# Performance work log

Measured on AMD Instinct MI355X. Metric: run time of the kernel, lower is better.

## Reference

```python
import jax, jax.numpy as jnp
import numpy as np
import math

B, L, D = 2, 2048, 512
H, HD = 8, 64                      # num_heads, head_dim = D // H
NG = D * (D - 1) // 2              # SO(D) generator count = 130816


def setup_inputs() -> dict:
    key = jax.random.key(0)
    ks = jax.random.split(key, 8)
    x = jax.random.normal(ks[0], (B, L, D), jnp.float32)
    # additive causal mask [L, L]
    mask = jnp.where(jnp.tril(jnp.ones((L, L), bool)), 0.0, -1e9).astype(jnp.float32)
    coef = lambda k: jax.random.normal(k, (NG,), jnp.float32) * 0.1
    basis = lambda k: jax.random.normal(k, (HD, HD), jnp.float32) * 0.1
    return {
        "x": x, "mask": mask,
        "coef_q": coef(ks[1]), "coef_k": coef(ks[2]),
        "coef_v": coef(ks[3]), "coef_o": coef(ks[4]),
        "bias_q": jnp.zeros((D,), jnp.float32), "bias_k": jnp.zeros((D,), jnp.float32),
        "bias_v": jnp.zeros((D,), jnp.float32), "bias_o": jnp.zeros((D,), jnp.float32),
        "basis_q": basis(ks[5]), "basis_k": basis(ks[6]),
    }


def _make_W(coefs):
    # W = I + sum_i coef_i * G_i, with G_i the antisymmetric basis (row-major i<j).
    iu = jnp.triu_indices(D, k=1)
    A = jnp.zeros((D, D), coefs.dtype).at[iu].set(coefs)
    return A - A.T + jnp.eye(D, dtype=coefs.dtype)


def _proj(x, coefs, bias):
    # F.linear(x, W, b) = x @ W.T + b
    return x @ _make_W(coefs).T + bias


def _invariants(t, basis):
    # t: [B, H, L, HD] -> concat(norm, t @ basis.T)[..., :HD]
    norm = jnp.linalg.norm(t, axis=-1, keepdims=True)
    ip = jnp.einsum('bhld,nd->bhln', t, basis)
    return jnp.concatenate([norm, ip], axis=-1)[..., :HD]


def reference(x, mask, coef_q, coef_k, coef_v, coef_o,
              bias_q, bias_k, bias_v, bias_o, basis_q, basis_k):
    split = lambda t: t.reshape(B, L, H, HD).transpose(0, 2, 1, 3)  # [B,H,L,HD]
    Q = split(_proj(x, coef_q, bias_q))
    K = split(_proj(x, coef_k, bias_k))
    V = split(_proj(x, coef_v, bias_v))
    Qi = _invariants(Q, basis_q)
    Ki = _invariants(K, basis_k)
    scores = jnp.einsum('bhld,bhmd->bhlm', Qi, Ki) / math.sqrt(HD) + mask
    attn = jax.nn.softmax(scores, axis=-1)
    out = jnp.einsum('bhlm,bhmd->bhld', attn, V)
    out = out.transpose(0, 2, 1, 3).reshape(B, L, D)
    return _proj(out, coef_o, bias_o)
```

## Files before the change

kernel.cpp:

```cpp
#include <hip/hip_runtime.h>
#include <hip/hip_bf16.h>
#include <math.h>

#define D_ 512
#define B_ 2
#define L_ 2048
#define H_ 8
#define HD_ 64

typedef __attribute__((ext_vector_type(8))) short short8;
typedef __attribute__((ext_vector_type(4))) float f32x4;
typedef _Float16 half8 __attribute__((ext_vector_type(8)));

__device__ __forceinline__ ushort f2bf(float f) {
  __hip_bfloat16 h = __float2bfloat16(f);
  return *(ushort*)&h;
}
__device__ __forceinline__ float bf2f(ushort u) {
  unsigned int v = ((unsigned int)u) << 16;
  union { unsigned int u; float f; } c; c.u = v; return c.f;
}
__device__ __forceinline__ ushort f2h(float f) {
  _Float16 h = (_Float16)f;
  return *(ushort*)&h;
}
__device__ __forceinline__ int swz(int row, int col) {
  return row*64 + (((col>>3) ^ (row&7))<<3) + (col&7);
}
__device__ __forceinline__ int tri_idx(int i, int j) {
  return i*(D_-1) - (i*(i-1))/2 + (j - i - 1);
}

#define GLL16(g, l) __builtin_amdgcn_global_load_lds( \
    (const __attribute__((address_space(1))) void*)(g), \
    (__attribute__((address_space(3))) void*)(l), 16, 0, 0)

__global__ void prep_kernel(const float* __restrict__ x,
                            const float* __restrict__ cq, const float* __restrict__ ck,
                            const float* __restrict__ cv, const float* __restrict__ co,
                            const float* __restrict__ basq, const float* __restrict__ bask,
                            ushort* __restrict__ xb, ushort* __restrict__ Wb,
                            ushort* __restrict__ Bq, ushort* __restrict__ Bk) {
  int blk = blockIdx.x, tid = threadIdx.x;
  if (blk < 2048) {
    int i = (blk*256 + tid)*4;
    float4 v = *(const float4*)(x + i);
    ushort4 o = make_ushort4(f2h(v.x), f2h(v.y), f2h(v.z), f2h(v.w));
    *(ushort4*)(xb + i) = o;
  } else if (blk < 6144) {
    int e = (blk-2048)*256 + tid;
    int m = e >> 18, n = (e>>9)&511, k = e&511;
    const float* cf = (m==0)?cq:(m==1)?ck:(m==2)?cv:co;
    float v = (k>n) ? cf[tri_idx(n,k)] : (k<n) ? -cf[tri_idx(k,n)] : 0.f;
    Wb[e] = f2h(v);
  } else {
    int e = (blk-6144)*256 + tid;
    int which = e >> 12, ee = e & 4095;
    int n = ee >> 6, d = ee & 63;
    const float* bs = which ? bask : basq;
    float v = (n==0) ? 0.f : bs[(n-1)*64 + d];
    (which ? Bk : Bq)[ee] = f2h(v);
  }
}

__device__ __forceinline__ void stage_xw(const ushort* __restrict__ Xg,
                                         const ushort* __restrict__ Wqg,
                                         const ushort* __restrict__ Wkg,
                                         const ushort* __restrict__ Wvg,
                                         ushort* A, ushort* Q, ushort* K, ushort* V,
                                         int w, int lane) {
  const int r8 = lane >> 3;
  const int cx = (lane & 7) ^ r8;
  #pragma unroll
  for (int s = 0; s < 2; ++s) {
    const int seg = w*2 + s;
    const int row = seg*8 + r8;
    const size_t go = (size_t)row*512 + cx*8;
    GLL16(Xg  + go, (char*)A + seg*1024);
    GLL16(Wqg + go, (char*)Q + seg*1024);
    GLL16(Wkg + go, (char*)K + seg*1024);
    GLL16(Wvg + go, (char*)V + seg*1024);
  }
}

__global__ __launch_bounds__(256) void proj_qkv_kernel(
    const ushort* __restrict__ Xb, const float* __restrict__ Xf,
    const ushort* __restrict__ Wb,
    const float* __restrict__ bq, const float* __restrict__ bk,
    const float* __restrict__ bv,
    const ushort* __restrict__ Bq, const ushort* __restrict__ Bk,
    ushort* __restrict__ QiO, float* __restrict__ NqV,
    ushort* __restrict__ KiO, float* __restrict__ NkV,
    ushort* __restrict__ Vt_g, float* __restrict__ TileMax)
{
  __shared__ ushort BufA[2][4096];
  __shared__ ushort BufQ[2][4096];
  __shared__ ushort BufK[2][4096];
  __shared__ ushort BufV[2][4096];
  __shared__ float WaveMax[4];

  const int tid = threadIdx.x;
  const int lane = tid & 63, w = tid >> 6;
  const int lr = lane & 15, lg = lane >> 4;
  const int h = blockIdx.x, mb = blockIdx.y;
  const int n0 = h*64, m0 = mb*64;
  const ushort* Xg  = Xb + (size_t)m0*512;
  const ushort* Wqg = Wb + (size_t)n0*512;
  const ushort* Wkg = Wb + 262144 + (size_t)n0*512;
  const ushort* Wvg = Wb + 524288 + (size_t)n0*512;

  f32x4 accQ[4] = {}, accK[4] = {}, accV[4] = {};
  stage_xw(Xg, Wqg, Wkg, Wvg, BufA[0], BufQ[0], BufK[0], BufV[0], w, lane);

  for (int p = 0; p < 8; ++p) {
    const int cur = p & 1;
    if (p < 7) {
      const int k0 = (p+1)*64;
      stage_xw(Xg + k0, Wqg + k0, Wkg + k0, Wvg + k0,
               BufA[cur^1], BufQ[cur^1], BufK[cur^1], BufV[cur^1], w, lane);
      asm volatile("s_waitcnt vmcnt(8)" ::: "memory");
    } else {
      asm volatile("s_waitcnt vmcnt(0)" ::: "memory");
    }
    __builtin_amdgcn_sched_barrier(0);
    __builtin_amdgcn_s_barrier();
    __builtin_amdgcn_sched_barrier(0);

    half8 af[2];
    #pragma unroll
    for (int ks = 0; ks < 2; ++ks)
      af[ks] = *(const half8*)&BufA[cur][swz(w*16+lr, (ks*4+lg)*8)];
    #pragma unroll
    for (int nb = 0; nb < 4; ++nb) {
      #pragma unroll
      for (int ks = 0; ks < 2; ++ks) {
        int so = swz(nb*16+lr, (ks*4+lg)*8);
        accQ[nb] = __builtin_amdgcn_mfma_f32_16x16x32_f16(af[ks], *(const half8*)&BufQ[cur][so], accQ[nb], 0,0,0);
        accK[nb] = __builtin_amdgcn_mfma_f32_16x16x32_f16(af[ks], *(const half8*)&BufK[cur][so], accK[nb], 0,0,0);
        accV[nb] = __builtin_amdgcn_mfma_f32_16x16x32_f16(af[ks], *(const half8*)&BufV[cur][so], accV[nb], 0,0,0);
      }
    }
    __builtin_amdgcn_sched_barrier(0);
    __builtin_amdgcn_s_barrier();
    __builtin_amdgcn_sched_barrier(0);
  }

  float ex[4][4];
  #pragma unroll
  for (int nb = 0; nb < 4; ++nb)
    #pragma unroll
    for (int r = 0; r < 4; ++r) {
      size_t m = m0 + w*16 + lg*4 + r;
      ex[nb][r] = Xf[m*512 + n0 + nb*16 + lr];
    }
  const int b = m0 >> 11;

  #pragma unroll
  for (int nb = 0; nb < 4; ++nb) {
    float bv4 = bv[n0 + nb*16 + lr];
    float v0 = ex[nb][0] + accV[nb][0] + bv4;
    float v1 = ex[nb][1] + accV[nb][1] + bv4;
    float v2 = ex[nb][2] + accV[nb][2] + bv4;
    float v3 = ex[nb][3] + accV[nb][3] + bv4;
    ushort4 o = make_ushort4(f2bf(v0), f2bf(v1), f2bf(v2), f2bf(v3));
    int l0 = (m0 & 2047) + w*16 + lg*4;
    size_t idx = (size_t)(b*8 + h)*131072 + (size_t)(nb*16 + lr)*2048 + l0;
    *(ushort4*)(Vt_g + idx) = o;
  }

  float qQ[4][4], qK[4][4];
  #pragma unroll
  for (int nb = 0; nb < 4; ++nb) {
    float bq4 = bq[n0 + nb*16 + lr];
    float bk4 = bk[n0 + nb*16 + lr];
    #pragma unroll
    for (int r = 0; r < 4; ++r) {
      qQ[nb][r] = ex[nb][r] + accQ[nb][r] + bq4;
      qK[nb][r] = ex[nb][r] + accK[nb][r] + bk4;
    }
  }
  float normQ[4], normK[4];
  #pragma unroll
  for (int r = 0; r < 4; ++r) {
    float sq = 0.f, sk = 0.f;
    #pragma unroll
    for (int nb = 0; nb < 4; ++nb) {
      sq = fmaf(qQ[nb][r], qQ[nb][r], sq);
      sk = fmaf(qK[nb][r], qK[nb][r], sk);
    }
    sq += __shfl_xor(sq, 1, 16); sk += __shfl_xor(sk, 1, 16);
    sq += __shfl_xor(sq, 2, 16); sk += __shfl_xor(sk, 2, 16);
    sq += __shfl_xor(sq, 4, 16); sk += __shfl_xor(sk, 4, 16);
    sq += __shfl_xor(sq, 8, 16); sk += __shfl_xor(sk, 8, 16);
    normQ[r] = sqrtf(sq); normK[r] = sqrtf(sk);
  }
  __syncthreads();
  {
    #pragma unroll
    for (int i = 0; i < 2; ++i) {
      int idx = tid + 256*i;
      int row = idx >> 3, c = idx & 7;
      int so = swz(row, c*8);
      *(short8*)&BufQ[0][so] = *(const short8*)(Bq + row*64 + c*8);
      *(short8*)&BufK[0][so] = *(const short8*)(Bk + row*64 + c*8);
    }
  }
  #pragma unroll
  for (int nb = 0; nb < 4; ++nb)
    #pragma unroll
    for (int r = 0; r < 4; ++r) {
      int so = swz(w*16 + lg*4 + r, nb*16 + lr);
      BufA[0][so] = f2h(qQ[nb][r]);
      BufV[0][so] = f2h(qK[nb][r]);
    }
  __syncthreads();

  f32x4 acc2Q[4] = {}, acc2K[4] = {};
  half8 aq[2], ak[2];
  #pragma unroll
  for (int ks = 0; ks < 2; ++ks) {
    aq[ks] = *(const half8*)&BufA[0][swz(w*16+lr, (ks*4+lg)*8)];
    ak[ks] = *(const half8*)&BufV[0][swz(w*16+lr, (ks*4+lg)*8)];
  }
  #pragma unroll
  for (int nb = 0; nb < 4; ++nb) {
    #pragma unroll
    for (int ks = 0; ks < 2; ++ks) {
      int so = swz(nb*16+lr, (ks*4+lg)*8);
      acc2Q[nb] = __builtin_amdgcn_mfma_f32_16x16x32_f16(aq[ks], *(const half8*)&BufQ[0][so], acc2Q[nb], 0,0,0);
      acc2K[nb] = __builtin_amdgcn_mfma_f32_16x16x32_f16(ak[ks], *(const half8*)&BufK[0][so], acc2K[nb], 0,0,0);
    }
  }

  float rnq[4] = {0.f,0.f,0.f,0.f}, rnk[4] = {0.f,0.f,0.f,0.f};
  #pragma unroll
  for (int nb = 0; nb < 4; ++nb)
    #pragma unroll
    for (int r = 0; r < 4; ++r) {
      int ninv = nb*16 + lr;
      int l = (m0 & 2047) + w*16 + lg*4 + r;
      float vq = (ninv == 0) ? normQ[r] : acc2Q[nb][r];
      vq *= 0.125f;
      rnq[r] = fmaf(vq, vq, rnq[r]);
      QiO[((size_t)(b*8 + h)*2048 + l)*64 + ninv] = f2h(vq);
      float vk = (ninv == 0) ? normK[r] : acc2K[nb][r];
      rnk[r] = fmaf(vk, vk, rnk[r]);
      KiO[((size_t)(b*8 + h)*2048 + l)*64 + ninv] = f2h(vk);
    }
  float kmax = -1e30f;
  #pragma unroll
  for (int r = 0; r < 4; ++r) {
    float sq = rnq[r], sk = rnk[r];
    sq += __shfl_xor(sq, 1, 16); sk += __shfl_xor(sk, 1, 16);
    sq += __shfl_xor(sq, 2, 16); sk += __shfl_xor(sk, 2, 16);
    sq += __shfl_xor(sq, 4, 16); sk += __shfl_xor(sk, 4, 16);
    sq += __shfl_xor(sq, 8, 16); sk += __shfl_xor(sk, 8, 16);
    float nk = sqrtf(sk);
    kmax = fmaxf(kmax, nk);
    if (lr == 0) {
      int l = (m0 & 2047) + w*16 + lg*4 + r;
      NqV[(size_t)(b*8 + h)*2048 + l] = sqrtf(sq);
      NkV[(size_t)(b*8 + h)*2048 + l] = nk;
    }
  }
  kmax = fmaxf(kmax, __shfl_xor(kmax, 16));
  kmax = fmaxf(kmax, __shfl_xor(kmax, 32));
  if (lane == 0) WaveMax[w] = kmax;
  __syncthreads();
  if (tid == 0) {
    float m01 = fmaxf(WaveMax[0], WaveMax[1]);
    float m23 = fmaxf(WaveMax[2], WaveMax[3]);
    TileMax[(b*8 + h)*32 + (mb & 31)] = fmaxf(m01, m23);
  }
}

__device__ __forceinline__ void stage_kv(const ushort* __restrict__ Kg,
                                         const ushort* __restrict__ Vg,
                                         ushort* KB, ushort* VB,
                                         int w, int lane) {
  const int r8 = lane >> 3;
  const int cx = (lane & 7) ^ r8;
  #pragma unroll
  for (int s = 0; s < 2; ++s) {
    const int seg = w*2 + s;
    const int row = seg*8 + r8;
    GLL16(Kg + (size_t)row*64 + cx*8,   (char*)KB + seg*1024);
    GLL16(Vg + (size_t)row*2048 + cx*8, (char*)VB + seg*1024);
  }
}

__global__ __launch_bounds__(256) void attn_kernel(
    const ushort* __restrict__ Qi_g, const float* __restrict__ NqV,
    const ushort* __restrict__ Ki_g, const float* __restrict__ TileMax,
    const ushort* __restrict__ Vt_g,
    float* __restrict__ PartO, float* __restrict__ PartL)
{
  __shared__ ushort KS[2][4096], VS[2][4096], Pl[4096];

  const int tid = threadIdx.x;
  const int lane = tid & 63, w = tid >> 6;
  const int lr = lane & 15, lg = lane >> 4;
  const int blk = blockIdx.x;
  const int bh = ((blk & 7) << 1) | ((blk >> 3) & 1);
  const int gh = blk >> 4;
  const int g  = gh & 31;
  const int half = gh >> 5;
  const int qb = (g < 16) ? (31 - g) : (g - 16);
  const int T = qb + 1, mid = (T + 1) >> 1;
  const int lo = half ? mid : 0, hi = half ? T : mid;
  const ushort* Kg0 = Ki_g + (size_t)bh*131072;
  const ushort* Vg0 = Vt_g + (size_t)bh*131072;
  const int qg0 = qb*64;
  const int qloc = w*16 + lr;
  const int prow = qloc;

  const size_t qoff = ((size_t)bh*2048 + qg0 + qloc)*64;
  const half8 qf0 = *(const half8*)(Qi_g + qoff + lg*8);
  const half8 qf1 = *(const half8*)(Qi_g + qoff + 32 + lg*8);
  const float nqv = NqV[(size_t)bh*2048 + qg0 + qloc];

  float mk = (lane <= qb) ? TileMax[bh*32 + lane] : -1e30f;
  #pragma unroll
  for (int off = 1; off < 64; off <<= 1) mk = fmaxf(mk, __shfl_xor(mk, off));
  const float m_ub = nqv * mk;

  float l_lane = 0.f;
  f32x4 accO[4] = {};

  if (lo < hi)
    stage_kv(Kg0 + (size_t)lo*4096, Vg0 + lo*64, KS[lo&1], VS[lo&1], w, lane);

  for (int jb = lo; jb < hi; ++jb) {
    const int cur = jb & 1;
    if (jb + 1 < hi) {
      stage_kv(Kg0 + (size_t)(jb+1)*4096, Vg0 + (jb+1)*64,
               KS[cur^1], VS[cur^1], w, lane);
      asm volatile("s_waitcnt vmcnt(4)" ::: "memory");
    } else {
      asm volatile("s_waitcnt vmcnt(0)" ::: "memory");
    }
    __builtin_amdgcn_sched_barrier(0);
    __builtin_amdgcn_s_barrier();
    __builtin_amdgcn_sched_barrier(0);

    f32x4 sf[4];
    #pragma unroll
    for (int cb = 0; cb < 4; ++cb) {
      f32x4 a = {0.f,0.f,0.f,0.f};
      half8 k0 = *(const half8*)&KS[cur][swz(cb*16+lr, lg*8)];
      half8 k1 = *(const half8*)&KS[cur][swz(cb*16+lr, (4+lg)*8)];
      a = __builtin_amdgcn_mfma_f32_16x16x32_f16(k0, qf0, a, 0,0,0);
      a = __builtin_amdgcn_mfma_f32_16x16x32_f16(k1, qf1, a, 0,0,0);
      sf[cb] = a;
    }
    if (jb == qb) {
      #pragma unroll
      for (int cb = 0; cb < 4; ++cb)
        #pragma unroll
        for (int r = 0; r < 4; ++r)
          if (cb*16 + lg*4 + r > qloc) sf[cb][r] = -1e30f;
    }

    #pragma unroll
    for (int cb = 0; cb < 4; ++cb)
      #pragma unroll
      for (int r = 0; r < 4; ++r) {
        float p = __expf(sf[cb][r] - m_ub);
        l_lane += p;
        sf[cb][r] = p;
      }
    #pragma unroll
    for (int cb = 0; cb < 4; ++cb) {
      ushort4 pk = make_ushort4(f2bf(sf[cb][0]), f2bf(sf[cb][1]),
                                f2bf(sf[cb][2]), f2bf(sf[cb][3]));
      *(ushort4*)&Pl[swz(prow, cb*16 + lg*4)] = pk;
    }

    short8 pfr[2];
    #pragma unroll
    for (int ks = 0; ks < 2; ++ks)
      pfr[ks] = *(const short8*)&Pl[swz(prow, (ks*4+lg)*8)];
    #pragma unroll
    for (int db = 0; db < 4; ++db) {
      f32x4 a = accO[db];
      short8 v0 = *(const short8*)&VS[cur][swz(db*16+lr, lg*8)];
      short8 v1 = *(const short8*)&VS[cur][swz(db*16+lr, (4+lg)*8)];
      a = __builtin_amdgcn_mfma_f32_16x16x32_bf16(v0, pfr[0], a, 0,0,0);
      a = __builtin_amdgcn_mfma_f32_16x16x32_bf16(v1, pfr[1], a, 0,0,0);
      accO[db] = a;
    }

    __builtin_amdgcn_sched_barrier(0);
    __builtin_amdgcn_s_barrier();
    __builtin_amdgcn_sched_barrier(0);
  }

  l_lane += __shfl_xor(l_lane, 16);
  l_lane += __shfl_xor(l_lane, 32);
  const int pbase = half*512 + bh*32 + qb;
  #pragma unroll
  for (int db = 0; db < 4; ++db)
    *(f32x4*)(PartO + (size_t)pbase*4096 + qloc*64 + db*16 + lg*4) = accO[db];
  if (lg == 0) PartL[pbase*64 + qloc] = l_lane;
}

__global__ __launch_bounds__(256) void proj_o_kernel(
    const float* __restrict__ PartO, const float* __restrict__ PartL,
    const ushort* __restrict__ Wb, const float* __restrict__ bo,
    float* __restrict__ OutF)
{
  __shared__ ushort BufA[4096];
  __shared__ ushort BufB[4096];
  __shared__ float ExactT[64][65];

  const int tid = threadIdx.x;
  const int lane = tid & 63, w = tid >> 6;
  const int lr = lane & 15, lg = lane >> 4;
  const int h = blockIdx.x, mb = blockIdx.y;
  const int n0 = h*64, m0 = mb*64;
  const ushort* Wm = Wb + 3*262144;
  const int b_ = m0 >> 11;
  const int qb_ = (m0 & 2047) >> 6;

  float4 r0a[2], r0b[2], r1a[2], r1b[2];
  float rl0[2], rl1[2];
  short8 rw[2];

  auto issue = [&](int p) {
    const int bh_ = b_*8 + p;
    const size_t pb0 = (size_t)(bh_*32 + qb_)*4096;
    const int lbase = (bh_*32 + qb_)*64;
    #pragma unroll
    for (int i = 0; i < 2; ++i) {
      int idx = tid + 256*i;
      int row = idx >> 3, c = idx & 7;
      rl0[i] = PartL[lbase + row];
      rl1[i] = PartL[32768 + lbase + row];
      const float* s0 = PartO + pb0 + row*64 + c*8;
      r0a[i] = *(const float4*)s0;
      r0b[i] = *(const float4*)(s0 + 4);
      r1a[i] = *(const float4*)(s0 + 2097152);
      r1b[i] = *(const float4*)(s0 + 2097152 + 4);
      rw[i] = *(const short8*)(Wm + (size_t)(n0+row)*512 + p*64 + c*8);
    }
  };

  issue(0);
  f32x4 acc[4] = {};
  for (int p = 0; p < 8; ++p) {
    __syncthreads();
    #pragma unroll
    for (int i = 0; i < 2; ++i) {
      int idx = tid + 256*i;
      int row = idx >> 3, c = idx & 7;
      float inv = 1.0f / (rl0[i] + rl1[i]);
      float o[8] = {(r0a[i].x+r1a[i].x)*inv, (r0a[i].y+r1a[i].y)*inv,
                    (r0a[i].z+r1a[i].z)*inv, (r0a[i].w+r1a[i].w)*inv,
                    (r0b[i].x+r1b[i].x)*inv, (r0b[i].y+r1b[i].y)*inv,
                    (r0b[i].z+r1b[i].z)*inv, (r0b[i].w+r1b[i].w)*inv};
      if (p == h) {
        #pragma unroll
        for (int k = 0; k < 8; ++k) ExactT[row][c*8+k] = o[k];
      }
      ushort u[8];
      #pragma unroll
      for (int k = 0; k < 8; ++k) u[k] = f2h(o[k]);
      *(short8*)&BufA[swz(row, c*8)] = *(short8*)u;
      *(short8*)&BufB[swz(row, c*8)] = rw[i];
    }
    if (p < 7) issue(p+1);
    __syncthreads();
    half8 af[2];
    #pragma unroll
    for (int ks = 0; ks < 2; ++ks)
      af[ks] = *(const half8*)&BufA[swz(w*16+lr, (ks*4+lg)*8)];
    #pragma unroll
    for (int nb = 0; nb < 4; ++nb) {
      #pragma unroll
      for (int ks = 0; ks < 2; ++ks) {
        half8 bfr = *(const half8*)&BufB[swz(nb*16+lr, (ks*4+lg)*8)];
        acc[nb] = __builtin_amdgcn_mfma_f32_16x16x32_f16(af[ks], bfr, acc[nb], 0,0,0);
      }
    }
  }

  #pragma unroll
  for (int nb = 0; nb < 4; ++nb) {
    float bo4 = bo[n0 + nb*16 + lr];
    #pragma unroll
    for (int r = 0; r < 4; ++r) {
      int row = w*16 + lg*4 + r;
      size_t m = m0 + row;
      OutF[m*512 + n0 + nb*16 + lr] = ExactT[row][nb*16 + lr] + acc[nb][r] + bo4;
    }
  }
}

extern "C" void kernel_launch(void* const* d_in, const int* in_sizes, int n_in,
                              void* d_out, int out_size, void* d_ws, size_t ws_size,
                              hipStream_t stream) {
  const float* x       = (const float*)d_in[0];
  const float* coef_q  = (const float*)d_in[2];
  const float* coef_k  = (const float*)d_in[3];
  const float* coef_v  = (const float*)d_in[4];
  const float* coef_o  = (const float*)d_in[5];
  const float* bias_q  = (const float*)d_in[6];
  const float* bias_k  = (const float*)d_in[7];
  const float* bias_v  = (const float*)d_in[8];
  const float* bias_o  = (const float*)d_in[9];
  const float* basis_q = (const float*)d_in[10];
  const float* basis_k = (const float*)d_in[11];
  float* out = (float*)d_out;

  ushort* xb    = (ushort*)d_ws;
  ushort* Wb    = xb + 2097152;
  ushort* Bq    = Wb + 1048576;
  ushort* Bk    = Bq + 4096;
  ushort* Qi    = Bk + 4096;
  ushort* Ki    = Qi + 2097152;
  ushort* Vt_g  = Ki + 2097152;
  float*  NqV   = (float*)(Vt_g + 2097152);
  float*  NkV   = NqV + 32768;
  float*  PartO = NkV + 32768;
  float*  PartL = PartO + 4194304;
  float*  TileMax = PartL + 65536;

  prep_kernel<<<dim3(6176), 256, 0, stream>>>(x, coef_q, coef_k, coef_v, coef_o,
                                              basis_q, basis_k, xb, Wb, Bq, Bk);

  proj_qkv_kernel<<<dim3(8, 64), 256, 0, stream>>>(xb, x, Wb,
      bias_q, bias_k, bias_v, Bq, Bk, Qi, NqV, Ki, NkV, Vt_g, TileMax);

  attn_kernel<<<dim3(1024), 256, 0, stream>>>(Qi, NqV, Ki, TileMax, Vt_g,
                                              PartO, PartL);

  proj_o_kernel<<<dim3(8, 64), 256, 0, stream>>>(PartO, PartL, Wb, bias_o, out);
}
```

Baseline: 75.99 us.

## Process two KV tiles per iteration with a four-deep shared-memory ring

The attention loop now handles two 64-key tiles per iteration and keeps four KV buffers in LDS, prefetching two tiles ahead. This halves the number of block-wide barriers per key and gives the scheduler two independent score/exp chains to interleave, aiming to hide load and MFMA latency. In exchange, LDS use roughly doubles (about 72KB per block), which can lower occupancy, and register pressure rises. An odd remaining tile is handled in a separate tail.

```diff
diff --git a/kernel.cpp b/kernel.cpp
--- a/kernel.cpp
+++ b/kernel.cpp
@@ -295,7 +295,7 @@
     const ushort* __restrict__ Vt_g,
     float* __restrict__ PartO, float* __restrict__ PartL)
 {
-  __shared__ ushort KS[2][4096], VS[2][4096], Pl[4096];
+  __shared__ ushort KS[4][4096], VS[4][4096], Pl[4096];
 
   const int tid = threadIdx.x;
   const int lane = tid & 63, w = tid >> 6;
@@ -328,27 +328,137 @@
   f32x4 accO[4] = {};
 
   if (lo < hi)
-    stage_kv(Kg0 + (size_t)lo*4096, Vg0 + lo*64, KS[lo&1], VS[lo&1], w, lane);
-
-  for (int jb = lo; jb < hi; ++jb) {
-    const int cur = jb & 1;
-    if (jb + 1 < hi) {
-      stage_kv(Kg0 + (size_t)(jb+1)*4096, Vg0 + (jb+1)*64,
-               KS[cur^1], VS[cur^1], w, lane);
-      asm volatile("s_waitcnt vmcnt(4)" ::: "memory");
-    } else {
-      asm volatile("s_waitcnt vmcnt(0)" ::: "memory");
-    }
+    stage_kv(Kg0 + (size_t)lo*4096, Vg0 + lo*64, KS[lo&3], VS[lo&3], w, lane);
+  if (lo + 1 < hi)
+    stage_kv(Kg0 + (size_t)(lo+1)*4096, Vg0 + (lo+1)*64,
+             KS[(lo+1)&3], VS[(lo+1)&3], w, lane);
+
+  int jb = lo;
+  for (; jb + 1 < hi; jb += 2) {
+    int nst = 0;
+    if (jb + 2 < hi) {
+      stage_kv(Kg0 + (size_t)(jb+2)*4096, Vg0 + (jb+2)*64,
+               KS[(jb+2)&3], VS[(jb+2)&3], w, lane);
+      ++nst;
+    }
+    if (jb + 3 < hi) {
+      stage_kv(Kg0 + (size_t)(jb+3)*4096, Vg0 + (jb+3)*64,
+               KS[(jb+3)&3], VS[(jb+3)&3], w, lane);
+      ++nst;
+    }
+    if (nst == 2)      asm volatile("s_waitcnt vmcnt(8)" ::: "memory");
+    else if (nst == 1) asm volatile("s_waitcnt vmcnt(4)" ::: "memory");
+    else               asm volatile("s_waitcnt vmcnt(0)" ::: "memory");
     __builtin_amdgcn_sched_barrier(0);
     __builtin_amdgcn_s_barrier();
     __builtin_amdgcn_sched_barrier(0);
 
-    f32x4 sf[4];
+    const ushort* KA = KS[jb & 3];
+    const ushort* VA = VS[jb & 3];
+    const ushort* KB = KS[(jb+1) & 3];
+    const ushort* VB = VS[(jb+1) & 3];
+
+    f32x4 sfA[4], sfB[4];
     #pragma unroll
     for (int cb = 0; cb < 4; ++cb) {
       f32x4 a = {0.f,0.f,0.f,0.f};
-      half8 k0 = *(const half8*)&KS[cur][swz(cb*16+lr, lg*8)];
-      half8 k1 = *(const half8*)&KS[cur][swz(cb*16+lr, (4+lg)*8)];
+      half8 k0 = *(const half8*)&KA[swz(cb*16+lr, lg*8)];
+      half8 k1 = *(const half8*)&KA[swz(cb*16+lr, (4+lg)*8)];
+      a = __builtin_amdgcn_mfma_f32_16x16x32_f16(k0, qf0, a, 0,0,0);
+      a = __builtin_amdgcn_mfma_f32_16x16x32_f16(k1, qf1, a, 0,0,0);
+      sfA[cb] = a;
+      f32x4 b2 = {0.f,0.f,0.f,0.f};
+      half8 k2 = *(const half8*)&KB[swz(cb*16+lr, lg*8)];
+      half8 k3 = *(const half8*)&KB[swz(cb*16+lr, (4+lg)*8)];
+      b2 = __builtin_amdgcn_mfma_f32_16x16x32_f16(k2, qf0, b2, 0,0,0);
+      b2 = __builtin_amdgcn_mfma_f32_16x16x32_f16(k3, qf1, b2, 0,0,0);
+      sfB[cb] = b2;
+    }
+    if (jb == qb) {
+      #pragma unroll
+      for (int cb = 0; cb < 4; ++cb)
+        #pragma unroll
+        for (int r = 0; r < 4; ++r)
+          if (cb*16 + lg*4 + r > qloc) sfA[cb][r] = -1e30f;
+    }
+    if (jb + 1 == qb) {
+      #pragma unroll
+      for (int cb = 0; cb < 4; ++cb)
+        #pragma unroll
+        for (int r = 0; r < 4; ++r)
+          if (cb*16 + lg*4 + r > qloc) sfB[cb][r] = -1e30f;
+    }
+
+    #pragma unroll
+    for (int cb = 0; cb < 4; ++cb)
+      #pragma unroll
+      for (int r = 0; r < 4; ++r) {
+        float p = __expf(sfA[cb][r] - m_ub);
+        l_lane += p;
+        sfA[cb][r] = p;
+      }
+    #pragma unroll
+    for (int cb = 0; cb < 4; ++cb)
+      #pragma unroll
+      for (int r = 0; r < 4; ++r) {
+        float p = __expf(sfB[cb][r] - m_ub);
+        l_lane += p;
+        sfB[cb][r] = p;
+      }
+
+    #pragma unroll
+    for (int cb = 0; cb < 4; ++cb) {
+      ushort4 pk = make_ushort4(f2bf(sfA[cb][0]), f2bf(sfA[cb][1]),
+                                f2bf(sfA[cb][2]), f2bf(sfA[cb][3]));
+      *(ushort4*)&Pl[swz(prow, cb*16 + lg*4)] = pk;
+    }
+    short8 pfrA[2];
+    #pragma unroll
+    for (int ks = 0; ks < 2; ++ks)
+      pfrA[ks] = *(const short8*)&Pl[swz(prow, (ks*4+lg)*8)];
+    #pragma unroll
+    for (int cb = 0; cb < 4; ++cb) {
+      ushort4 pk = make_ushort4(f2bf(sfB[cb][0]), f2bf(sfB[cb][1]),
+                                f2bf(sfB[cb][2]), f2bf(sfB[cb][3]));
+      *(ushort4*)&Pl[swz(prow, cb*16 + lg*4)] = pk;
+    }
+    short8 pfrB[2];
+    #pragma unroll
+    for (int ks = 0; ks < 2; ++ks)
+      pfrB[ks] = *(const short8*)&Pl[swz(prow, (ks*4+lg)*8)];
+
+    #pragma unroll
+    for (int db = 0; db < 4; ++db) {
+      f32x4 a = accO[db];
+      short8 v0 = *(const short8*)&VA[swz(db*16+lr, lg*8)];
+      short8 v1 = *(const short8*)&VA[swz(db*16+lr, (4+lg)*8)];
+      a = __builtin_amdgcn_mfma_f32_16x16x32_bf16(v0, pfrA[0], a, 0,0,0);
+      a = __builtin_amdgcn_mfma_f32_16x16x32_bf16(v1, pfrA[1], a, 0,0,0);
+      short8 v2 = *(const short8*)&VB[swz(db*16+lr, lg*8)];
+      short8 v3 = *(const short8*)&VB[swz(db*16+lr, (4+lg)*8)];
+      a = __builtin_amdgcn_mfma_f32_16x16x32_bf16(v2, pfrB[0], a, 0,0,0);
+      a = __builtin_amdgcn_mfma_f32_16x16x32_bf16(v3, pfrB[1], a, 0,0,0);
+      accO[db] = a;
+    }
+
+    __builtin_amdgcn_sched_barrier(0);
+    __builtin_amdgcn_s_barrier();
+    __builtin_amdgcn_sched_barrier(0);
+  }
+
+  if (jb < hi) {
+    asm volatile("s_waitcnt vmcnt(0)" ::: "memory");
+    __builtin_amdgcn_sched_barrier(0);
+    __builtin_amdgcn_s_barrier();
+    __builtin_amdgcn_sched_barrier(0);
+    const ushort* KA = KS[jb & 3];
+    const ushort* VA = VS[jb & 3];
+    f32x4 sf[4];
+    #pragma unroll
+    for (int cb = 0; cb < 4; ++cb) {
+      f32x4 a = {0.f,0.f,0.f,0.f};
+      half8 k0 = *(const half8*)&KA[swz(cb*16+lr, lg*8)];
+      half8 k1 = *(const half8*)&KA[swz(cb*16+lr, (4+lg)*8)];
       a = __builtin_amdgcn_mfma_f32_16x16x32_f16(k0, qf0, a, 0,0,0);
       a = __builtin_amdgcn_mfma_f32_16x16x32_f16(k1, qf1, a, 0,0,0);
       sf[cb] = a;
@@ -360,7 +470,6 @@
         for (int r = 0; r < 4; ++r)
           if (cb*16 + lg*4 + r > qloc) sf[cb][r] = -1e30f;
     }
-
     #pragma unroll
     for (int cb = 0; cb < 4; ++cb)
       #pragma unroll
@@ -375,7 +484,6 @@
                                 f2bf(sf[cb][2]), f2bf(sf[cb][3]));
       *(ushort4*)&Pl[swz(prow, cb*16 + lg*4)] = pk;
     }
-
     short8 pfr[2];
     #pragma unroll
     for (int ks = 0; ks < 2; ++ks)
@@ -383,16 +491,12 @@
     #pragma unroll
     for (int db = 0; db < 4; ++db) {
       f32x4 a = accO[db];
-      short8 v0 = *(const short8*)&VS[cur][swz(db*16+lr, lg*8)];
-      short8 v1 = *(const short8*)&VS[cur][swz(db*16+lr, (4+lg)*8)];
+      short8 v0 = *(const short8*)&VA[swz(db*16+lr, lg*8)];
+      short8 v1 = *(const short8*)&VA[swz(db*16+lr, (4+lg)*8)];
       a = __builtin_amdgcn_mfma_f32_16x16x32_bf16(v0, pfr[0], a, 0,0,0);
       a = __builtin_amdgcn_mfma_f32_16x16x32_bf16(v1, pfr[1], a, 0,0,0);
       accO[db] = a;
     }
-
-    __builtin_amdgcn_sched_barrier(0);
-    __builtin_amdgcn_s_barrier();
-    __builtin_amdgcn_sched_barrier(0);
   }
 
   l_lane += __shfl_xor(l_lane, 16);
```

Result: no change. 76.75 us (+1.0%).

## Share staged K/V tiles across two query blocks per 512-thread workgroup

Applied to the files above, without the earlier changes.

The attention kernel now runs 512 threads per block. Each block handles a pair of adjacent 64-row query blocks (8 waves), and both share the same double-buffered K/V tiles in shared memory, which roughly halves the K/V global loads and LDS staging per query row. The split into two partial halves is re-derived per pair, and the lower query block masks out tiles beyond its diagonal. Those masked tiles still cost full MFMA work and barriers, and the larger blocks reduce the count of independent workgroups.

```diff
diff --git a/kernel.cpp b/kernel.cpp
--- a/kernel.cpp
+++ b/kernel.cpp
@@ -274,52 +274,48 @@
   }
 }
 
-__device__ __forceinline__ void stage_kv(const ushort* __restrict__ Kg,
-                                         const ushort* __restrict__ Vg,
-                                         ushort* KB, ushort* VB,
-                                         int w, int lane) {
+__device__ __forceinline__ void stage_kv8(const ushort* __restrict__ Kg,
+                                          const ushort* __restrict__ Vg,
+                                          ushort* KB, ushort* VB,
+                                          int w, int lane) {
   const int r8 = lane >> 3;
   const int cx = (lane & 7) ^ r8;
-  #pragma unroll
-  for (int s = 0; s < 2; ++s) {
-    const int seg = w*2 + s;
-    const int row = seg*8 + r8;
-    GLL16(Kg + (size_t)row*64 + cx*8,   (char*)KB + seg*1024);
-    GLL16(Vg + (size_t)row*2048 + cx*8, (char*)VB + seg*1024);
-  }
-}
-
-__global__ __launch_bounds__(256) void attn_kernel(
+  const int row = w*8 + r8;
+  GLL16(Kg + (size_t)row*64 + cx*8,   (char*)KB + w*1024);
+  GLL16(Vg + (size_t)row*2048 + cx*8, (char*)VB + w*1024);
+}
+
+__global__ __launch_bounds__(512) void attn_kernel(
     const ushort* __restrict__ Qi_g, const float* __restrict__ NqV,
     const ushort* __restrict__ Ki_g, const float* __restrict__ TileMax,
     const ushort* __restrict__ Vt_g,
     float* __restrict__ PartO, float* __restrict__ PartL)
 {
-  __shared__ ushort KS[2][4096], VS[2][4096], Pl[4096];
+  __shared__ ushort KS[2][4096], VS[2][4096], Pl[8][1024];
 
   const int tid = threadIdx.x;
   const int lane = tid & 63, w = tid >> 6;
   const int lr = lane & 15, lg = lane >> 4;
   const int blk = blockIdx.x;
   const int bh = ((blk & 7) << 1) | ((blk >> 3) & 1);
-  const int gh = blk >> 4;
-  const int g  = gh & 31;
-  const int half = gh >> 5;
-  const int qb = (g < 16) ? (31 - g) : (g - 16);
-  const int T = qb + 1, mid = (T + 1) >> 1;
-  const int lo = half ? mid : 0, hi = half ? T : mid;
+  const int rest = blk >> 4;
+  const int rr = rest & 15;
+  const int half = rest >> 4;
+  const int qt = half ? (15 - rr) : rr;
+  const int qbw = 2*qt + (w >> 2);
+  const int lo = half ? (qt + 1) : 0;
+  const int hi = half ? (2*qt + 2) : (qt + 1);
   const ushort* Kg0 = Ki_g + (size_t)bh*131072;
   const ushort* Vg0 = Vt_g + (size_t)bh*131072;
-  const int qg0 = qb*64;
-  const int qloc = w*16 + lr;
-  const int prow = qloc;
-
-  const size_t qoff = ((size_t)bh*2048 + qg0 + qloc)*64;
+  const int qloc = (w & 3)*16 + lr;
+  ushort* Plw = Pl[w];
+
+  const size_t qoff = ((size_t)bh*2048 + qbw*64 + qloc)*64;
   const half8 qf0 = *(const half8*)(Qi_g + qoff + lg*8);
   const half8 qf1 = *(const half8*)(Qi_g + qoff + 32 + lg*8);
-  const float nqv = NqV[(size_t)bh*2048 + qg0 + qloc];
-
-  float mk = (lane <= qb) ? TileMax[bh*32 + lane] : -1e30f;
+  const float nqv = NqV[(size_t)bh*2048 + qbw*64 + qloc];
+
+  float mk = (lane <= qbw) ? TileMax[bh*32 + lane] : -1e30f;
   #pragma unroll
   for (int off = 1; off < 64; off <<= 1) mk = fmaxf(mk, __shfl_xor(mk, off));
   const float m_ub = nqv * mk;
@@ -328,14 +324,14 @@
   f32x4 accO[4] = {};
 
   if (lo < hi)
-    stage_kv(Kg0 + (size_t)lo*4096, Vg0 + lo*64, KS[lo&1], VS[lo&1], w, lane);
+    stage_kv8(Kg0 + (size_t)lo*4096, Vg0 + lo*64, KS[lo&1], VS[lo&1], w, lane);
 
   for (int jb = lo; jb < hi; ++jb) {
     const int cur = jb & 1;
     if (jb + 1 < hi) {
-      stage_kv(Kg0 + (size_t)(jb+1)*4096, Vg0 + (jb+1)*64,
-               KS[cur^1], VS[cur^1], w, lane);
-      asm volatile("s_waitcnt vmcnt(4)" ::: "memory");
+      stage_kv8(Kg0 + (size_t)(jb+1)*4096, Vg0 + (jb+1)*64,
+                KS[cur^1], VS[cur^1], w, lane);
+      asm volatile("s_waitcnt vmcnt(2)" ::: "memory");
     } else {
       asm volatile("s_waitcnt vmcnt(0)" ::: "memory");
     }
@@ -353,12 +349,18 @@
       a = __builtin_amdgcn_mfma_f32_16x16x32_f16(k1, qf1, a, 0,0,0);
       sf[cb] = a;
     }
-    if (jb == qb) {
+    if (jb == qbw) {
       #pragma unroll
       for (int cb = 0; cb < 4; ++cb)
         #pragma unroll
         for (int r = 0; r < 4; ++r)
           if (cb*16 + lg*4 + r > qloc) sf[cb][r] = -1e30f;
+    } else if (jb > qbw) {
+      #pragma unroll
+      for (int cb = 0; cb < 4; ++cb)
+        #pragma unroll
+        for (int r = 0; r < 4; ++r)
+          sf[cb][r] = -1e30f;
     }
 
     #pragma unroll
@@ -373,13 +375,13 @@
     for (int cb = 0; cb < 4; ++cb) {
       ushort4 pk = make_ushort4(f2bf(sf[cb][0]), f2bf(sf[cb][1]),
                                 f2bf(sf[cb][2]), f2bf(sf[cb][3]));
-      *(ushort4*)&Pl[swz(prow, cb*16 + lg*4)] = pk;
+      *(ushort4*)&Plw[swz(lr, cb*16 + lg*4)] = pk;
     }
 
     short8 pfr[2];
     #pragma unroll
     for (int ks = 0; ks < 2; ++ks)
-      pfr[ks] = *(const short8*)&Pl[swz(prow, (ks*4+lg)*8)];
+      pfr[ks] = *(const short8*)&Plw[swz(lr, (ks*4+lg)*8)];
     #pragma unroll
     for (int db = 0; db < 4; ++db) {
       f32x4 a = accO[db];
@@ -397,7 +399,7 @@
 
   l_lane += __shfl_xor(l_lane, 16);
   l_lane += __shfl_xor(l_lane, 32);
-  const int pbase = half*512 + bh*32 + qb;
+  const int pbase = half*512 + bh*32 + qbw;
   #pragma unroll
   for (int db = 0; db < 4; ++db)
     *(f32x4*)(PartO + (size_t)pbase*4096 + qloc*64 + db*16 + lg*4) = accO[db];
@@ -531,8 +533,8 @@
   proj_qkv_kernel<<<dim3(8, 64), 256, 0, stream>>>(xb, x, Wb,
       bias_q, bias_k, bias_v, Bq, Bk, Qi, NqV, Ki, NkV, Vt_g, TileMax);
 
-  attn_kernel<<<dim3(1024), 256, 0, stream>>>(Qi, NqV, Ki, TileMax, Vt_g,
-                                              PartO, PartL);
+  attn_kernel<<<dim3(512), 512, 0, stream>>>(Qi, NqV, Ki, TileMax, Vt_g,
+                                             PartO, PartL);
 
   proj_o_kernel<<<dim3(8, 64), 256, 0, stream>>>(PartO, PartL, Wb, bias_o, out);
 }
```

New measurement: 76.21 us. About the same (+0.3%).

## Run attention blocks as single wave handling all 64 query rows

Applied to the files above, without the earlier changes.

The attention kernel drops from four waves per block to one wave that processes all four 16-row query slices. K/V fragments are loaded into registers once per tile and reused across the four slices, and the per-tile block barriers are removed because one wave does all the staging and compute. In exchange, register pressure rises a lot (16 accumulator tiles plus 16 score tiles), which may cut occupancy or cause spills. Each block now has a quarter of the threads to issue loads and hide latency, and LDS per block is unchanged.

```diff
diff --git a/kernel.cpp b/kernel.cpp
--- a/kernel.cpp
+++ b/kernel.cpp
@@ -274,31 +274,28 @@
   }
 }
 
-__device__ __forceinline__ void stage_kv(const ushort* __restrict__ Kg,
-                                         const ushort* __restrict__ Vg,
-                                         ushort* KB, ushort* VB,
-                                         int w, int lane) {
+__device__ __forceinline__ void stage_kv1(const ushort* __restrict__ Kg,
+                                          const ushort* __restrict__ Vg,
+                                          ushort* KB, ushort* VB, int lane) {
   const int r8 = lane >> 3;
   const int cx = (lane & 7) ^ r8;
   #pragma unroll
-  for (int s = 0; s < 2; ++s) {
-    const int seg = w*2 + s;
+  for (int seg = 0; seg < 8; ++seg) {
     const int row = seg*8 + r8;
     GLL16(Kg + (size_t)row*64 + cx*8,   (char*)KB + seg*1024);
     GLL16(Vg + (size_t)row*2048 + cx*8, (char*)VB + seg*1024);
   }
 }
 
-__global__ __launch_bounds__(256) void attn_kernel(
+__global__ __launch_bounds__(64) void attn_kernel(
     const ushort* __restrict__ Qi_g, const float* __restrict__ NqV,
     const ushort* __restrict__ Ki_g, const float* __restrict__ TileMax,
     const ushort* __restrict__ Vt_g,
     float* __restrict__ PartO, float* __restrict__ PartL)
 {
-  __shared__ ushort KS[2][4096], VS[2][4096], Pl[4096];
-
-  const int tid = threadIdx.x;
-  const int lane = tid & 63, w = tid >> 6;
+  __shared__ ushort KS[2][4096], VS[2][4096], Pl[4][1024];
+
+  const int lane = threadIdx.x & 63;
   const int lr = lane & 15, lg = lane >> 4;
   const int blk = blockIdx.x;
   const int bh = ((blk & 7) << 1) | ((blk >> 3) & 1);
@@ -310,98 +307,116 @@
   const int lo = half ? mid : 0, hi = half ? T : mid;
   const ushort* Kg0 = Ki_g + (size_t)bh*131072;
   const ushort* Vg0 = Vt_g + (size_t)bh*131072;
-  const int qg0 = qb*64;
-  const int qloc = w*16 + lr;
-  const int prow = qloc;
-
-  const size_t qoff = ((size_t)bh*2048 + qg0 + qloc)*64;
-  const half8 qf0 = *(const half8*)(Qi_g + qoff + lg*8);
-  const half8 qf1 = *(const half8*)(Qi_g + qoff + 32 + lg*8);
-  const float nqv = NqV[(size_t)bh*2048 + qg0 + qloc];
+
+  half8 qf[4][2];
+  float nqv[4];
+  #pragma unroll
+  for (int i = 0; i < 4; ++i) {
+    const size_t qoff = ((size_t)bh*2048 + qb*64 + i*16 + lr)*64;
+    qf[i][0] = *(const half8*)(Qi_g + qoff + lg*8);
+    qf[i][1] = *(const half8*)(Qi_g + qoff + 32 + lg*8);
+    nqv[i] = NqV[(size_t)bh*2048 + qb*64 + i*16 + lr];
+  }
 
   float mk = (lane <= qb) ? TileMax[bh*32 + lane] : -1e30f;
   #pragma unroll
   for (int off = 1; off < 64; off <<= 1) mk = fmaxf(mk, __shfl_xor(mk, off));
-  const float m_ub = nqv * mk;
-
-  float l_lane = 0.f;
-  f32x4 accO[4] = {};
+  float m_ub[4];
+  #pragma unroll
+  for (int i = 0; i < 4; ++i) m_ub[i] = nqv[i] * mk;
+
+  float l[4] = {0.f, 0.f, 0.f, 0.f};
+  f32x4 accO[4][4] = {};
 
   if (lo < hi)
-    stage_kv(Kg0 + (size_t)lo*4096, Vg0 + lo*64, KS[lo&1], VS[lo&1], w, lane);
+    stage_kv1(Kg0 + (size_t)lo*4096, Vg0 + lo*64, KS[lo&1], VS[lo&1], lane);
 
   for (int jb = lo; jb < hi; ++jb) {
     const int cur = jb & 1;
     if (jb + 1 < hi) {
-      stage_kv(Kg0 + (size_t)(jb+1)*4096, Vg0 + (jb+1)*64,
-               KS[cur^1], VS[cur^1], w, lane);
-      asm volatile("s_waitcnt vmcnt(4)" ::: "memory");
+      stage_kv1(Kg0 + (size_t)(jb+1)*4096, Vg0 + (jb+1)*64,
+                KS[cur^1], VS[cur^1], lane);
+      asm volatile("s_waitcnt vmcnt(16)" ::: "memory");
     } else {
       asm volatile("s_waitcnt vmcnt(0)" ::: "memory");
     }
     __builtin_amdgcn_sched_barrier(0);
-    __builtin_amdgcn_s_barrier();
-    __builtin_amdgcn_sched_barrier(0);
-
-    f32x4 sf[4];
+
+    half8 kf[4][2];
+    short8 vf[4][2];
     #pragma unroll
     for (int cb = 0; cb < 4; ++cb) {
-      f32x4 a = {0.f,0.f,0.f,0.f};
-      half8 k0 = *(const half8*)&KS[cur][swz(cb*16+lr, lg*8)];
-      half8 k1 = *(const half8*)&KS[cur][swz(cb*16+lr, (4+lg)*8)];
-      a = __builtin_amdgcn_mfma_f32_16x16x32_f16(k0, qf0, a, 0,0,0);
-      a = __builtin_amdgcn_mfma_f32_16x16x32_f16(k1, qf1, a, 0,0,0);
-      sf[cb] = a;
-    }
+      kf[cb][0] = *(const half8*)&KS[cur][swz(cb*16+lr, lg*8)];
+      kf[cb][1] = *(const half8*)&KS[cur][swz(cb*16+lr, (4+lg)*8)];
+      vf[cb][0] = *(const short8*)&VS[cur][swz(cb*16+lr, lg*8)];
+      vf[cb][1] = *(const short8*)&VS[cur][swz(cb*16+lr, (4+lg)*8)];
+    }
+
+    f32x4 sf[4][4];
+    #pragma unroll
+    for (int i = 0; i < 4; ++i)
+      #pragma unroll
+      for (int cb = 0; cb < 4; ++cb) {
+        f32x4 a = {0.f,0.f,0.f,0.f};
+        a = __builtin_amdgcn_mfma_f32_16x16x32_f16(kf[cb][0], qf[i][0], a, 0,0,0);
+        a = __builtin_amdgcn_mfma_f32_16x16x32_f16(kf[cb][1], qf[i][1], a, 0,0,0);
+        sf[i][cb] = a;
+      }
     if (jb == qb) {
+      #pragma unroll
+      for (int i = 0; i < 4; ++i)
+        #pragma unroll
+        for (int cb = 0; cb < 4; ++cb)
+          #pragma unroll
+          for (int r = 0; r < 4; ++r)
+            if (cb*16 + lg*4 + r > i*16 + lr) sf[i][cb][r] = -1e30f;
+    }
+
+    #pragma unroll
+    for (int i = 0; i < 4; ++i)
       #pragma unroll
       for (int cb = 0; cb < 4; ++cb)
         #pragma unroll
-        for (int r = 0; r < 4; ++r)
-          if (cb*16 + lg*4 + r > qloc) sf[cb][r] = -1e30f;
-    }
-
-    #pragma unroll
-    for (int cb = 0; cb < 4; ++cb)
-      #pragma unroll
-      for (int r = 0; r < 4; ++r) {
-        float p = __expf(sf[cb][r] - m_ub);
-        l_lane += p;
-        sf[cb][r] = p;
+        for (int r = 0; r < 4; ++r) {
+          float p = __expf(sf[i][cb][r] - m_ub[i]);
+          l[i] += p;
+          sf[i][cb][r] = p;
+        }
+
+    #pragma unroll
+    for (int i = 0; i < 4; ++i)
+      #pragma unroll
+      for (int cb = 0; cb < 4; ++cb) {
+        ushort4 pk = make_ushort4(f2bf(sf[i][cb][0]), f2bf(sf[i][cb][1]),
+                                  f2bf(sf[i][cb][2]), f2bf(sf[i][cb][3]));
+        *(ushort4*)&Pl[i][swz(lr, cb*16 + lg*4)] = pk;
       }
     #pragma unroll
-    for (int cb = 0; cb < 4; ++cb) {
-      ushort4 pk = make_ushort4(f2bf(sf[cb][0]), f2bf(sf[cb][1]),
-                                f2bf(sf[cb][2]), f2bf(sf[cb][3]));
-      *(ushort4*)&Pl[swz(prow, cb*16 + lg*4)] = pk;
-    }
-
-    short8 pfr[2];
-    #pragma unroll
-    for (int ks = 0; ks < 2; ++ks)
-      pfr[ks] = *(const short8*)&Pl[swz(prow, (ks*4+lg)*8)];
-    #pragma unroll
-    for (int db = 0; db < 4; ++db) {
-      f32x4 a = accO[db];
-      short8 v0 = *(const short8*)&VS[cur][swz(db*16+lr, lg*8)];
-      short8 v1 = *(const short8*)&VS[cur][swz(db*16+lr, (4+lg)*8)];
-      a = __builtin_amdgcn_mfma_f32_16x16x32_bf16(v0, pfr[0], a, 0,0,0);
-      a = __builtin_amdgcn_mfma_f32_16x16x32_bf16(v1, pfr[1], a, 0,0,0);
-      accO[db] = a;
-    }
-
-    __builtin_amdgcn_sched_barrier(0);
-    __builtin_amdgcn_s_barrier();
-    __builtin_amdgcn_sched_barrier(0);
-  }
-
-  l_lane += __shfl_xor(l_lane, 16);
-  l_lane += __shfl_xor(l_lane, 32);
+    for (int i = 0; i < 4; ++i) {
+      short8 p0 = *(const short8*)&Pl[i][swz(lr, lg*8)];
+      short8 p1 = *(const short8*)&Pl[i][swz(lr, (4+lg)*8)];
+      #pragma unroll
+      for (int db = 0; db < 4; ++db) {
+        f32x4 a = accO[i][db];
+        a = __builtin_amdgcn_mfma_f32_16x16x32_bf16(vf[db][0], p0, a, 0,0,0);
+        a = __builtin_amdgcn_mfma_f32_16x16x32_bf16(vf[db][1], p1, a, 0,0,0);
+        accO[i][db] = a;
+      }
+    }
+  }
+
   const int pbase = half*512 + bh*32 + qb;
   #pragma unroll
-  for (int db = 0; db < 4; ++db)
-    *(f32x4*)(PartO + (size_t)pbase*4096 + qloc*64 + db*16 + lg*4) = accO[db];
-  if (lg == 0) PartL[pbase*64 + qloc] = l_lane;
+  for (int i = 0; i < 4; ++i) {
+    float li = l[i];
+    li += __shfl_xor(li, 16);
+    li += __shfl_xor(li, 32);
+    const int qloc = i*16 + lr;
+    #pragma unroll
+    for (int db = 0; db < 4; ++db)
+      *(f32x4*)(PartO + (size_t)pbase*4096 + qloc*64 + db*16 + lg*4) = accO[i][db];
+    if (lg == 0) PartL[pbase*64 + qloc] = li;
+  }
 }
 
 __global__ __launch_bounds__(256) void proj_o_kernel(
@@ -531,8 +546,8 @@
   proj_qkv_kernel<<<dim3(8, 64), 256, 0, stream>>>(xb, x, Wb,
       bias_q, bias_k, bias_v, Bq, Bk, Qi, NqV, Ki, NkV, Vt_g, TileMax);
 
-  attn_kernel<<<dim3(1024), 256, 0, stream>>>(Qi, NqV, Ki, TileMax, Vt_g,
-                                              PartO, PartL);
+  attn_kernel<<<dim3(1024), 64, 0, stream>>>(Qi, NqV, Ki, TileMax, Vt_g,
+                                             PartO, PartL);
 
   proj_o_kernel<<<dim3(8, 64), 256, 0, stream>>>(PartO, PartL, Wb, bias_o, out);
 }
```

Result: slower. 92.33 us (+21.5%).
